# Performance work log

Measured on AMD Instinct MI355X. Metric: run time of the kernel, lower is better.

Reference implementation:

```python
import jax, jax.numpy as jnp
import numpy as np
from jax import lax

B, C, H, W = 4, 256, 64, 64
NH, DK, DV = 8, 32, 32
KER, PAD = 3, 1


def conv1x1(x, w, b=None):
    # x: [B,C,H,W], w: [O,C] (1x1 conv kernel), b: [O] or None
    y = jnp.einsum('bchw,oc->bohw', x, w)
    if b is not None:
        y = y + b[None, :, None, None]
    return y


def unfold(x, k, pad):
    # F.unfold equivalent: [B,C,H,W] -> [B, C*k*k, H, W] (channel-major patch order)
    return lax.conv_general_dilated_patches(x, (k, k), (1, 1), [(pad, pad), (pad, pad)])


def local_attention(q, k, v, kernel, pad, n_head):
    # per-head local windowed attention over a kernel x kernel neighborhood
    b, c, h, w = q.shape
    d = c // n_head
    kk = kernel * kernel
    qh = q.reshape(b, n_head, d, h, w)
    kpat = unfold(k, kernel, pad).reshape(b, n_head, d, kk, h, w)
    vpat = unfold(v, kernel, pad).reshape(b, n_head, d, kk, h, w)
    scale = 1.0 / np.sqrt(float(d)).astype(np.float32)
    logits = jnp.einsum('bhdxy,bhdkxy->bhkxy', qh, kpat) * scale
    attn = jax.nn.softmax(logits, axis=2)
    out = jnp.einsum('bhkxy,bhdkxy->bhdxy', attn, vpat)
    return out.reshape(b, c, h, w)


def layernorm2d(x, g, b, eps=1e-6):
    mu = jnp.mean(x, axis=1, keepdims=True)
    var = jnp.mean((x - mu) ** 2, axis=1, keepdims=True)
    return (x - mu) / jnp.sqrt(var + eps) * g[None, :, None, None] + b[None, :, None, None]


def batchnorm2d(x, g, b, eps=1e-5):
    mu = jnp.mean(x, axis=(0, 2, 3), keepdims=True)
    var = jnp.mean((x - mu) ** 2, axis=(0, 2, 3), keepdims=True)
    return (x - mu) / jnp.sqrt(var + eps) * g[None, :, None, None] + b[None, :, None, None]


def mha(xq, xkv, wq, wk, wv, wfc, g, bias, kernel, pad):
    residual = xq
    q = conv1x1(xq, wq)
    k = conv1x1(xkv, wk)
    v = conv1x1(xkv, wv)
    o = local_attention(q, k, v, kernel, pad, NH)
    o = conv1x1(o, wfc) + residual
    return layernorm2d(o, g, bias)


def ffn(x, w1, b1, w2, b2, g, bias):
    residual = x
    y = conv1x1(jax.nn.relu(conv1x1(x, w1, b1)), w2, b2)
    y = batchnorm2d(y, g, bias)
    return y + residual


def setup_inputs() -> dict:
    key = jax.random.key(0)
    ks = jax.random.split(key, 16)
    s = 0.05
    d = {
        'input1': jax.random.normal(ks[0], (B, C, H, W), jnp.float32),
        'input2': jax.random.normal(ks[1], (B, C, H, W), jnp.float32),
        'slf_wq': jax.random.normal(ks[2], (NH * DK, C), jnp.float32) * s,
        'slf_wk': jax.random.normal(ks[3], (NH * DK, C), jnp.float32) * s,
        'slf_wv': jax.random.normal(ks[4], (NH * DV, C), jnp.float32) * s,
        'slf_fc': jax.random.normal(ks[5], (C, NH * DV), jnp.float32) * s,
        'slf_g': jnp.ones((C,), jnp.float32),
        'slf_b': jnp.zeros((C,), jnp.float32),
        'crs_wq': jax.random.normal(ks[6], (NH * DK, C), jnp.float32) * s,
        'crs_wk': jax.random.normal(ks[7], (NH * DK, C), jnp.float32) * s,
        'crs_wv': jax.random.normal(ks[8], (NH * DV, C), jnp.float32) * s,
        'crs_fc': jax.random.normal(ks[9], (C, NH * DV), jnp.float32) * s,
        'crs_g': jnp.ones((C,), jnp.float32),
        'crs_b': jnp.zeros((C,), jnp.float32),
        'ffn_w1': jax.random.normal(ks[10], (C, C), jnp.float32) * s,
        'ffn_b1': jnp.zeros((C,), jnp.float32),
        'ffn_w2': jax.random.normal(ks[11], (C, C), jnp.float32) * s,
        'ffn_b2': jnp.zeros((C,), jnp.float32),
        'ffn_bn_g': jnp.ones((C,), jnp.float32),
        'ffn_bn_b': jnp.zeros((C,), jnp.float32),
        'kernel': KER,
        'pad': PAD,
    }
    return d


def reference(input1, input2, slf_wq, slf_wk, slf_wv, slf_fc, slf_g, slf_b,
              crs_wq, crs_wk, crs_wv, crs_fc, crs_g, crs_b,
              ffn_w1, ffn_b1, ffn_w2, ffn_b2, ffn_bn_g, ffn_bn_b, kernel, pad):
    slf1 = mha(input1, input1, slf_wq, slf_wk, slf_wv, slf_fc, slf_g, slf_b, kernel, pad)
    slf2 = mha(input2, input2, slf_wq, slf_wk, slf_wv, slf_fc, slf_g, slf_b, kernel, pad)
    crs1 = mha(slf1, slf2, crs_wq, crs_wk, crs_wv, crs_fc, crs_g, crs_b, kernel, pad)
    crs2 = mha(slf2, slf1, crs_wq, crs_wk, crs_wv, crs_fc, crs_g, crs_b, kernel, pad)
    out1 = ffn(crs1, ffn_w1, ffn_b1, ffn_w2, ffn_b2, ffn_bn_g, ffn_bn_b)
    out2 = ffn(crs2, ffn_w1, ffn_b1, ffn_w2, ffn_b2, ffn_bn_g, ffn_bn_b)
    return (out1, out2)
```

## Files before the change

kernel.cpp:

```cpp
#include <hip/hip_runtime.h>
#include <stdint.h>

using u16 = unsigned short;
typedef __bf16 bf16x8 __attribute__((ext_vector_type(8)));
typedef __bf16 bf16x2 __attribute__((ext_vector_type(2)));
typedef float f32x4 __attribute__((ext_vector_type(4)));

#define NPIX 16384
#define CDIM 256

__device__ __forceinline__ float b2f(u16 u) {
  union { unsigned i; float f; } c; c.i = ((unsigned)u) << 16; return c.f;
}
__device__ __forceinline__ u16 f2b(float x) {
  union { __bf16 h; u16 u; } c; c.h = (__bf16)x; return c.u;
}
__device__ __forceinline__ unsigned pack2(float a, float b) {
  union { bf16x2 v; unsigned u; } c; c.v[0] = (__bf16)a; c.v[1] = (__bf16)b; return c.u;
}
__device__ __forceinline__ void unpack8(uint4 w, float* f) {
  f[0] = b2f((u16)(w.x & 0xffffu)); f[1] = b2f((u16)(w.x >> 16));
  f[2] = b2f((u16)(w.y & 0xffffu)); f[3] = b2f((u16)(w.y >> 16));
  f[4] = b2f((u16)(w.z & 0xffffu)); f[5] = b2f((u16)(w.z >> 16));
  f[6] = b2f((u16)(w.w & 0xffffu)); f[7] = b2f((u16)(w.w >> 16));
}

__device__ __forceinline__ void async16(u16* l, const u16* g) {
  __builtin_amdgcn_global_load_lds((const __attribute__((address_space(1))) void*)g,
                                   (__attribute__((address_space(3))) void*)l, 16, 0, 0);
}

template <int NI, int NT>
__device__ __forceinline__ void stage_swz(u16* lds, const u16* src, int tid) {
#pragma unroll
  for (int i = 0; i < NI; ++i) {
    const int idx = i * NT + tid;
    const int row = idx >> 3;
    const int c8 = (idx & 7) ^ (row & 7);
    async16(lds + idx * 8, src + (size_t)row * 256 + c8 * 8);
  }
}

__device__ __forceinline__ void compute_tile(const u16* ab, const u16* bb,
                                             f32x4 (&acc)[4][4], int wr, int wc,
                                             int l15, int l4, int sw) {
#pragma unroll
  for (int kk = 0; kk < 2; ++kk) {
    const int cs = ((kk * 4 + l4) ^ sw) * 8;
    bf16x8 af[4], bfr[4];
#pragma unroll
    for (int mi = 0; mi < 4; ++mi)
      af[mi] = *(const bf16x8*)&ab[(wr * 64 + mi * 16 + l15) * 64 + cs];
#pragma unroll
    for (int ni = 0; ni < 4; ++ni)
      bfr[ni] = *(const bf16x8*)&bb[(wc * 64 + ni * 16 + l15) * 64 + cs];
#pragma unroll
    for (int mi = 0; mi < 4; ++mi)
#pragma unroll
      for (int ni = 0; ni < 4; ++ni)
        acc[mi][ni] = __builtin_amdgcn_mfma_f32_16x16x32_bf16(af[mi], bfr[ni],
                                                              acc[mi][ni], 0, 0, 0);
  }
}

__global__ void prep(const float* __restrict__ x1, const float* __restrict__ x2,
                     u16* __restrict__ X1, u16* __restrict__ X2,
                     const float* s0, const float* s1, const float* s2,
                     const float* s3, const float* s4, const float* s5,
                     const float* s6, const float* s7, const float* s8,
                     const float* s9, u16* __restrict__ wdst,
                     float* __restrict__ stats) {
  const int t = threadIdx.x;
  const int yy = blockIdx.y;
  if (yy >= 32) {
    const int m = yy - 32;
    if (m == 0 && blockIdx.x == 0) {
      ((float4*)stats)[t] = float4{0.f, 0.f, 0.f, 0.f};
    }
    const float* s;
    switch (m) {
      case 0: s = s0; break; case 1: s = s1; break; case 2: s = s2; break;
      case 3: s = s3; break; case 4: s = s4; break; case 5: s = s5; break;
      case 6: s = s6; break; case 7: s = s7; break; case 8: s = s8; break;
      default: s = s9; break;
    }
    const int i = (blockIdx.x * 256 + t) * 4;
    float4 v = *(const float4*)(s + i);
    uint2 o;
    o.x = pack2(v.x, v.y);
    o.y = pack2(v.z, v.w);
    *(uint2*)(wdst + (size_t)m * 65536 + i) = o;
    return;
  }
  __shared__ u16 tile[64][65];
  const int z = yy >> 2;
  const float* x = (z < 4) ? x1 : x2;
  u16* X = (z < 4) ? X1 : X2;
  const int b = z & 3, c0 = (yy & 3) * 64, hw0 = blockIdx.x * 64;
  {
    const int hw_l = t & 63, cb = t >> 6;
#pragma unroll
    for (int i = 0; i < 16; ++i) {
      const int c_l = cb * 16 + i;
      tile[c_l][hw_l] = f2b(x[((size_t)(b * 256 + c0 + c_l)) * 4096 + hw0 + hw_l]);
    }
  }
  __syncthreads();
  {
    const int c_l = t & 63, hb = t >> 6;
#pragma unroll
    for (int i = 0; i < 16; ++i) {
      const int hw_l = hb * 16 + i;
      X[((size_t)(b * 4096 + hw0 + hw_l)) * 256 + c0 + c_l] = tile[c_l][hw_l];
    }
  }
}

struct PG { const u16* X[6]; const u16* W[3]; u16* D[6]; };

__global__ void gemm_qkv(PG a) {
  __shared__ u16 As[2][8192];
  __shared__ u16 Bs[2][8192];
  const int tid = threadIdx.x;
  const int wave = tid >> 6, lane = tid & 63;
  const int p0 = blockIdx.x * 128;
  const int g = blockIdx.y >> 1, o0 = (blockIdx.y & 1) * 128;
  const int z = blockIdx.z;
  const u16* X = a.X[z * 3 + g];
  const u16* W = a.W[g];
  u16* D = a.D[z * 3 + g];
  const int wr = wave & 1, wc = wave >> 1;
  const int l15 = lane & 15, l4 = lane >> 4;
  const int sw = l15 & 7;
  f32x4 acc[4][4] = {};

  const u16* Xp = X + (size_t)p0 * 256;
  const u16* Wp = W + (size_t)o0 * 256;
  stage_swz<4, 256>(As[0], Xp, tid);
  stage_swz<4, 256>(Bs[0], Wp, tid);
  __syncthreads();

  for (int kt = 0; kt < 4; ++kt) {
    const int cur = kt & 1;
    if (kt < 3) {
      stage_swz<4, 256>(As[cur ^ 1], Xp + (kt + 1) * 64, tid);
      stage_swz<4, 256>(Bs[cur ^ 1], Wp + (kt + 1) * 64, tid);
    }
    compute_tile(As[cur], Bs[cur], acc, wr, wc, l15, l4, sw);
    __syncthreads();
  }
#pragma unroll
  for (int ni = 0; ni < 4; ++ni) {
    const int o = o0 + wc * 64 + ni * 16 + l15;
#pragma unroll
    for (int mi = 0; mi < 4; ++mi)
#pragma unroll
      for (int r = 0; r < 4; ++r) {
        const int p = p0 + wr * 64 + mi * 16 + l4 * 4 + r;
        D[(size_t)p * 256 + o] = f2b(acc[mi][ni][r]);
      }
  }
}

struct Paf { const u16* Q[2]; const u16* K[2]; const u16* V[2];
             const u16* res[2]; u16* dst[2];
             const u16* W; const float* g; const float* b; };

__global__ __launch_bounds__(512) void attn_fc_ln(Paf a) {
  __shared__ u16 A4[2][8192];
  __shared__ u16 Bs[16384];
  __shared__ float red[2][128][4];
  const int tid = threadIdx.x;
  const int wave = tid >> 6, lane = tid & 63;
  const int wr = wave & 1, wc = wave >> 1;
  const int l15 = lane & 15, l4 = lane >> 4;
  const int sw = l15 & 7;
  const int p0 = blockIdx.x * 128;
  const int z = blockIdx.y;
  const u16* __restrict__ Q = a.Q[z];
  const u16* __restrict__ K = a.K[z];
  const u16* __restrict__ V = a.V[z];
  const u16* __restrict__ res = a.res[z];
  u16* dst = a.dst[z];

  const int p_l = tid >> 2, hh = tid & 3;
  const int p = p0 + p_l;
  const int yq = (p >> 6) & 63, xq = p & 63;

  bool inb[9];
  ptrdiff_t noff[9];
#pragma unroll
  for (int j = 0; j < 9; ++j) {
    const int dy = j / 3 - 1, dx = j % 3 - 1;
    inb[j] = ((unsigned)(yq + dy) < 64u) && ((unsigned)(xq + dx) < 64u);
    noff[j] = (ptrdiff_t)(dy * 64 + dx) * 256;
  }

  stage_swz<4, 512>(Bs, a.W, tid);
  __builtin_amdgcn_sched_barrier(0);

  f32x4 acc[4][4] = {};
  for (int h = 0; h < 2; ++h) {
    const int head = h * 4 + hh;
    const size_t base = (size_t)p * 256 + head * 32;
    float q[32];
    {
      const uint4* qp = (const uint4*)(Q + base);
#pragma unroll
      for (int i = 0; i < 4; ++i) { uint4 w = qp[i]; unpack8(w, q + i * 8); }
    }
    float accj[9];
#pragma unroll
    for (int j = 0; j < 9; ++j) accj[j] = 0.f;
#pragma unroll
    for (int i = 0; i < 4; ++i) {
      uint4 w[9];
#pragma unroll
      for (int j = 0; j < 9; ++j)
        if (inb[j]) w[j] = ((const uint4*)(K + base + noff[j]))[i];
#pragma unroll
      for (int j = 0; j < 9; ++j) {
        if (inb[j]) {
          float kf[8]; unpack8(w[j], kf);
#pragma unroll
          for (int d = 0; d < 8; ++d) accj[j] += q[i * 8 + d] * kf[d];
        }
      }
    }
    float lg[9];
    float mx = -1e30f;
#pragma unroll
    for (int j = 0; j < 9; ++j) {
      const float l = inb[j] ? accj[j] * 0.17677669529663687f : 0.f;
      lg[j] = l;
      mx = fmaxf(mx, l);
    }
    float pr[9], den = 0.f;
#pragma unroll
    for (int j = 0; j < 9; ++j) { pr[j] = __expf(lg[j] - mx); den += pr[j]; }
    float out[32];
#pragma unroll
    for (int d = 0; d < 32; ++d) out[d] = 0.f;
#pragma unroll
    for (int i = 0; i < 4; ++i) {
      uint4 w[9];
#pragma unroll
      for (int j = 0; j < 9; ++j)
        if (inb[j]) w[j] = ((const uint4*)(V + base + noff[j]))[i];
#pragma unroll
      for (int j = 0; j < 9; ++j) {
        if (inb[j]) {
          float vf[8]; unpack8(w[j], vf);
          const float pw = pr[j];
#pragma unroll
          for (int d = 0; d < 8; ++d) out[i * 8 + d] += pw * vf[d];
        }
      }
    }
    const float inv = 1.f / den;
#pragma unroll
    for (int i = 0; i < 4; ++i) {
      uint4 w;
      w.x = pack2(out[i * 8 + 0] * inv, out[i * 8 + 1] * inv);
      w.y = pack2(out[i * 8 + 2] * inv, out[i * 8 + 3] * inv);
      w.z = pack2(out[i * 8 + 4] * inv, out[i * 8 + 5] * inv);
      w.w = pack2(out[i * 8 + 6] * inv, out[i * 8 + 7] * inv);
      const int c8g = hh * 4 + i;
      const int sub = c8g >> 3, c8in = c8g & 7;
      *(uint4*)&A4[sub][p_l * 64 + ((c8in ^ (p_l & 7)) * 8)] = w;
    }

    __syncthreads();
    compute_tile(A4[0], Bs, acc, wr, wc, l15, l4, sw);
    __syncthreads();
    stage_swz<4, 512>(Bs, a.W + (h * 2 + 1) * 64, tid);
    __syncthreads();
    compute_tile(A4[1], Bs, acc, wr, wc, l15, l4, sw);
    __syncthreads();
    if (h == 0) {
      stage_swz<4, 512>(Bs, a.W + 2 * 64, tid);
      __builtin_amdgcn_sched_barrier(0);
    }
  }

#pragma unroll
  for (int mi = 0; mi < 4; ++mi) {
#pragma unroll
    for (int r = 0; r < 4; ++r) {
      const int pl = wr * 64 + mi * 16 + l4 * 4 + r;
      const int pp = p0 + pl;
      float s = 0.f, s2 = 0.f;
#pragma unroll
      for (int ni = 0; ni < 4; ++ni) {
        const int o = wc * 64 + ni * 16 + l15;
        float vv = acc[mi][ni][r] + b2f(res[(size_t)pp * 256 + o]);
        acc[mi][ni][r] = vv;
        s += vv; s2 += vv * vv;
      }
#pragma unroll
      for (int m = 1; m < 16; m <<= 1) {
        s += __shfl_xor(s, m); s2 += __shfl_xor(s2, m);
      }
      if (l15 == 0) { red[0][pl][wc] = s; red[1][pl][wc] = s2; }
    }
  }
  __syncthreads();

  float gv[4], bv[4];
#pragma unroll
  for (int ni = 0; ni < 4; ++ni) {
    const int o = wc * 64 + ni * 16 + l15;
    gv[ni] = a.g[o]; bv[ni] = a.b[o];
  }
#pragma unroll
  for (int mi = 0; mi < 4; ++mi) {
#pragma unroll
    for (int r = 0; r < 4; ++r) {
      const int pl = wr * 64 + mi * 16 + l4 * 4 + r;
      const float st = red[0][pl][0] + red[0][pl][1] + red[0][pl][2] + red[0][pl][3];
      const float s2t = red[1][pl][0] + red[1][pl][1] + red[1][pl][2] + red[1][pl][3];
      const float mu = st * (1.f / 256.f);
      const float var = s2t * (1.f / 256.f) - mu * mu;
      const float inv = rsqrtf(var + 1e-6f);
      const int pp = p0 + pl;
#pragma unroll
      for (int ni = 0; ni < 4; ++ni) {
        const int o = wc * 64 + ni * 16 + l15;
        dst[(size_t)pp * 256 + o] = f2b((acc[mi][ni][r] - mu) * inv * gv[ni] + bv[ni]);
      }
    }
  }
}

struct Pff { const u16* X[2]; u16* U[2]; float* st[2];
             const u16* W1; const float* b1; const u16* W2; const float* b2; };

__global__ __launch_bounds__(512) void ffn_fused(Pff a) {
  __shared__ u16 mid[4 * 8192];
  __shared__ u16 As[8192];
  __shared__ u16 Bs[16384];
  const int tid = threadIdx.x;
  const int wave = tid >> 6, lane = tid & 63;
  const int wr = wave & 1, wc = wave >> 1;
  const int l15 = lane & 15, l4 = lane >> 4;
  const int sw = l15 & 7;
  const int p0 = blockIdx.x * 128;
  const int z = blockIdx.y;
  const u16* X = a.X[z];
  u16* U = a.U[z];
  float* st = a.st[z];
  const u16* Xp = X + (size_t)p0 * 256;

  f32x4 acc1[4][4] = {};
  for (int kt = 0; kt < 4; ++kt) {
    stage_swz<2, 512>(As, Xp + kt * 64, tid);
    stage_swz<4, 512>(Bs, a.W1 + kt * 64, tid);
    __syncthreads();
    compute_tile(As, Bs, acc1, wr, wc, l15, l4, sw);
    __syncthreads();
  }
  {
    float bvv[4];
#pragma unroll
    for (int ni = 0; ni < 4; ++ni) bvv[ni] = a.b1[wc * 64 + ni * 16 + l15];
    u16* ml = mid + wc * 8192;
#pragma unroll
    for (int mi = 0; mi < 4; ++mi) {
#pragma unroll
      for (int r = 0; r < 4; ++r) {
        const int pl = wr * 64 + mi * 16 + l4 * 4 + r;
#pragma unroll
        for (int ni = 0; ni < 4; ++ni) {
          const int col = ni * 16 + l15;
          const int c8 = col >> 3;
          const u16 hv = f2b(fmaxf(acc1[mi][ni][r] + bvv[ni], 0.f));
          ml[pl * 64 + ((c8 ^ (pl & 7)) * 8) + (col & 7)] = hv;
        }
      }
    }
  }

  f32x4 acc2[4][4] = {};
  for (int kt = 0; kt < 4; ++kt) {
    __syncthreads();
    stage_swz<4, 512>(Bs, a.W2 + kt * 64, tid);
    __syncthreads();
    compute_tile(mid + kt * 8192, Bs, acc2, wr, wc, l15, l4, sw);
  }
#pragma unroll
  for (int ni = 0; ni < 4; ++ni) {
    const int o = wc * 64 + ni * 16 + l15;
    const float bvv = a.b2[o];
    float s = 0.f, s2 = 0.f;
#pragma unroll
    for (int mi = 0; mi < 4; ++mi) {
#pragma unroll
      for (int r = 0; r < 4; ++r) {
        const int p = p0 + wr * 64 + mi * 16 + l4 * 4 + r;
        const u16 hv = f2b(acc2[mi][ni][r] + bvv);
        U[(size_t)p * 256 + o] = hv;
        const float vr = b2f(hv); s += vr; s2 += vr * vr;
      }
    }
    s += __shfl_xor(s, 16); s2 += __shfl_xor(s2, 16);
    s += __shfl_xor(s, 32); s2 += __shfl_xor(s2, 32);
    if (l4 == 0) { atomicAdd(&st[o], s); atomicAdd(&st[256 + o], s2); }
  }
}

struct Pbn { const u16* U[2]; const u16* res[2]; const float* st[2];
             float* out[2]; const float* g; const float* b; };

__global__ void bn_apply(Pbn a) {
  __shared__ float tile[64][65];
  const int t = threadIdx.x;
  const int s = blockIdx.z >> 2, b = blockIdx.z & 3;
  const u16* __restrict__ U = a.U[s];
  const u16* __restrict__ res = a.res[s];
  const float* st = a.st[s];
  float* out = a.out[s];
  const int c0 = blockIdx.y * 64, hw0 = blockIdx.x * 64;
  {
    const int c_l = t & 63, hb = t >> 6;
    const int c = c0 + c_l;
    const float mu = st[c] * (1.f / 16384.f);
    const float var = st[256 + c] * (1.f / 16384.f) - mu * mu;
    const float sc = rsqrtf(var + 1e-5f) * a.g[c];
    const float sh = a.b[c] - mu * sc;
#pragma unroll
    for (int i = 0; i < 16; ++i) {
      const int hw_l = hb * 16 + i;
      const size_t p = (size_t)b * 4096 + hw0 + hw_l;
      const float u = b2f(U[p * 256 + c]);
      const float r = b2f(res[p * 256 + c]);
      tile[hw_l][c_l] = u * sc + sh + r;
    }
  }
  __syncthreads();
  {
    const int hw_l = t & 63, cb2 = t >> 6;
#pragma unroll
    for (int i = 0; i < 16; ++i) {
      const int c_l = cb2 * 16 + i;
      out[((size_t)(b * 256 + c0 + c_l)) * 4096 + hw0 + hw_l] = tile[hw_l][c_l];
    }
  }
}

extern "C" void kernel_launch(void* const* d_in, const int* in_sizes, int n_in,
                              void* d_out, int out_size, void* d_ws, size_t ws_size,
                              hipStream_t stream) {
  const float* input1 = (const float*)d_in[0];
  const float* input2 = (const float*)d_in[1];
  const float* slf_wq = (const float*)d_in[2];
  const float* slf_wk = (const float*)d_in[3];
  const float* slf_wv = (const float*)d_in[4];
  const float* slf_fc = (const float*)d_in[5];
  const float* slf_g  = (const float*)d_in[6];
  const float* slf_b  = (const float*)d_in[7];
  const float* crs_wq = (const float*)d_in[8];
  const float* crs_wk = (const float*)d_in[9];
  const float* crs_wv = (const float*)d_in[10];
  const float* crs_fc = (const float*)d_in[11];
  const float* crs_g  = (const float*)d_in[12];
  const float* crs_b  = (const float*)d_in[13];
  const float* ffn_w1 = (const float*)d_in[14];
  const float* ffn_b1 = (const float*)d_in[15];
  const float* ffn_w2 = (const float*)d_in[16];
  const float* ffn_b2 = (const float*)d_in[17];
  const float* bn_g   = (const float*)d_in[18];
  const float* bn_b   = (const float*)d_in[19];

  float* out = (float*)d_out;
  u16* ws = (u16*)d_ws;
  const size_t TS = (size_t)NPIX * CDIM;
  u16* b[10];
  for (int i = 0; i < 10; ++i) b[i] = ws + (size_t)i * TS;
  u16* wb = ws + 10 * TS;
  u16 *Wsq = wb,             *Wsk = wb + 65536,     *Wsv = wb + 2 * 65536,
      *Wsf = wb + 3 * 65536, *Wcq = wb + 4 * 65536, *Wck = wb + 5 * 65536,
      *Wcv = wb + 6 * 65536, *Wcf = wb + 7 * 65536, *W1 = wb + 8 * 65536,
      *W2 = wb + 9 * 65536;
  float* stats = (float*)(wb + 10 * 65536);

  const dim3 tb(256);

  prep<<<dim3(64, 42), tb, 0, stream>>>(input1, input2, b[0], b[1],
                                        slf_wq, slf_wk, slf_wv, slf_fc,
                                        crs_wq, crs_wk, crs_wv, crs_fc,
                                        ffn_w1, ffn_w2, wb, stats);

  PG sa;
  sa.X[0] = b[0]; sa.X[1] = b[0]; sa.X[2] = b[0];
  sa.X[3] = b[1]; sa.X[4] = b[1]; sa.X[5] = b[1];
  sa.W[0] = Wsq; sa.W[1] = Wsk; sa.W[2] = Wsv;
  sa.D[0] = b[4]; sa.D[1] = b[5]; sa.D[2] = b[6];
  sa.D[3] = b[7]; sa.D[4] = b[8]; sa.D[5] = b[9];
  gemm_qkv<<<dim3(NPIX / 128, 6, 2), tb, 0, stream>>>(sa);

  Paf f1;
  f1.Q[0] = b[4]; f1.K[0] = b[5]; f1.V[0] = b[6];
  f1.Q[1] = b[7]; f1.K[1] = b[8]; f1.V[1] = b[9];
  f1.res[0] = b[0]; f1.res[1] = b[1];
  f1.dst[0] = b[2]; f1.dst[1] = b[3];
  f1.W = Wsf; f1.g = slf_g; f1.b = slf_b;
  attn_fc_ln<<<dim3(NPIX / 128, 2), dim3(512), 0, stream>>>(f1);

  PG ca;
  ca.X[0] = b[2]; ca.X[1] = b[3]; ca.X[2] = b[3];
  ca.X[3] = b[3]; ca.X[4] = b[2]; ca.X[5] = b[2];
  ca.W[0] = Wcq; ca.W[1] = Wck; ca.W[2] = Wcv;
  ca.D[0] = b[4]; ca.D[1] = b[5]; ca.D[2] = b[6];
  ca.D[3] = b[7]; ca.D[4] = b[8]; ca.D[5] = b[9];
  gemm_qkv<<<dim3(NPIX / 128, 6, 2), tb, 0, stream>>>(ca);

  Paf f2;
  f2.Q[0] = b[4]; f2.K[0] = b[5]; f2.V[0] = b[6];
  f2.Q[1] = b[7]; f2.K[1] = b[8]; f2.V[1] = b[9];
  f2.res[0] = b[2]; f2.res[1] = b[3];
  f2.dst[0] = b[0]; f2.dst[1] = b[1];
  f2.W = Wcf; f2.g = crs_g; f2.b = crs_b;
  attn_fc_ln<<<dim3(NPIX / 128, 2), dim3(512), 0, stream>>>(f2);

  Pff ff;
  ff.X[0] = b[0]; ff.X[1] = b[1];
  ff.U[0] = b[4]; ff.U[1] = b[7];
  ff.st[0] = stats; ff.st[1] = stats + 512;
  ff.W1 = W1; ff.b1 = ffn_b1; ff.W2 = W2; ff.b2 = ffn_b2;
  ffn_fused<<<dim3(NPIX / 128, 2), dim3(512), 0, stream>>>(ff);

  Pbn bn;
  bn.U[0] = b[4]; bn.U[1] = b[7];
  bn.res[0] = b[0]; bn.res[1] = b[1];
  bn.st[0] = stats; bn.st[1] = stats + 512;
  bn.out[0] = out; bn.out[1] = out + TS;
  bn.g = bn_g; bn.b = bn_b;
  bn_apply<<<dim3(64, 4, 8), tb, 0, stream>>>(bn);
}
```

Baseline: 286.5 us.

## Fuse cross-attention Q projection into self-attn and FFN into cross-attn

```diff
diff --git a/kernel.cpp b/kernel.cpp
--- a/kernel.cpp
+++ b/kernel.cpp
@@ -118,6 +118,7 @@
 
 struct PG { const u16* X[6]; const u16* W[3]; u16* D[6]; };
 
+template <int NG>
 __global__ void gemm_qkv(PG a) {
   __shared__ u16 As[2][8192];
   __shared__ u16 Bs[2][8192];
@@ -126,9 +127,9 @@
   const int p0 = blockIdx.x * 128;
   const int g = blockIdx.y >> 1, o0 = (blockIdx.y & 1) * 128;
   const int z = blockIdx.z;
-  const u16* X = a.X[z * 3 + g];
+  const u16* X = a.X[z * NG + g];
   const u16* W = a.W[g];
-  u16* D = a.D[z * 3 + g];
+  u16* D = a.D[z * NG + g];
   const int wr = wave & 1, wc = wave >> 1;
   const int l15 = lane & 15, l4 = lane >> 4;
   const int sw = l15 & 7;
@@ -162,13 +163,14 @@
   }
 }
 
-struct Paf { const u16* Q[2]; const u16* K[2]; const u16* V[2];
-             const u16* res[2]; u16* dst[2];
-             const u16* W; const float* g; const float* b; };
-
-__global__ __launch_bounds__(512) void attn_fc_ln(Paf a) {
+struct Pas { const u16* Q[2]; const u16* K[2]; const u16* V[2];
+             const u16* res[2]; u16* dstS[2]; u16* dstQc[2];
+             const u16* Wfc; const u16* Wcq; const float* g; const float* b; };
+
+__global__ __launch_bounds__(512) void attn_s(Pas a) {
   __shared__ u16 A4[2][8192];
   __shared__ u16 Bs[16384];
+  __shared__ u16 S4[4][8192];
   __shared__ float red[2][128][4];
   const int tid = threadIdx.x;
   const int wave = tid >> 6, lane = tid & 63;
@@ -181,7 +183,8 @@
   const u16* __restrict__ K = a.K[z];
   const u16* __restrict__ V = a.V[z];
   const u16* __restrict__ res = a.res[z];
-  u16* dst = a.dst[z];
+  u16* dstS = a.dstS[z];
+  u16* dstQc = a.dstQc[z];
 
   const int p_l = tid >> 2, hh = tid & 3;
   const int p = p0 + p_l;
@@ -196,7 +199,7 @@
     noff[j] = (ptrdiff_t)(dy * 64 + dx) * 256;
   }
 
-  stage_swz<4, 512>(Bs, a.W, tid);
+  stage_swz<4, 512>(Bs, a.Wfc, tid);
   __builtin_amdgcn_sched_barrier(0);
 
   f32x4 acc[4][4] = {};
@@ -273,15 +276,18 @@
     __syncthreads();
     compute_tile(A4[0], Bs, acc, wr, wc, l15, l4, sw);
     __syncthreads();
-    stage_swz<4, 512>(Bs, a.W + (h * 2 + 1) * 64, tid);
+    stage_swz<4, 512>(Bs, a.Wfc + (h * 2 + 1) * 64, tid);
     __syncthreads();
     compute_tile(A4[1], Bs, acc, wr, wc, l15, l4, sw);
     __syncthreads();
     if (h == 0) {
-      stage_swz<4, 512>(Bs, a.W + 2 * 64, tid);
+      stage_swz<4, 512>(Bs, a.Wfc + 2 * 64, tid);
       __builtin_amdgcn_sched_barrier(0);
     }
   }
+
+  stage_swz<4, 512>(Bs, a.Wcq, tid);
+  __builtin_amdgcn_sched_barrier(0);
 
 #pragma unroll
   for (int mi = 0; mi < 4; ++mi) {
@@ -326,19 +332,46 @@
 #pragma unroll
       for (int ni = 0; ni < 4; ++ni) {
         const int o = wc * 64 + ni * 16 + l15;
-        dst[(size_t)pp * 256 + o] = f2b((acc[mi][ni][r] - mu) * inv * gv[ni] + bv[ni]);
-      }
-    }
-  }
-}
-
-struct Pff { const u16* X[2]; u16* U[2]; float* st[2];
-             const u16* W1; const float* b1; const u16* W2; const float* b2; };
-
-__global__ __launch_bounds__(512) void ffn_fused(Pff a) {
-  __shared__ u16 mid[4 * 8192];
-  __shared__ u16 As[8192];
+        const u16 hv = f2b((acc[mi][ni][r] - mu) * inv * gv[ni] + bv[ni]);
+        dstS[(size_t)pp * 256 + o] = hv;
+        const int c8 = (ni * 16 + l15) >> 3;
+        S4[wc][pl * 64 + ((c8 ^ (pl & 7)) * 8) + (l15 & 7)] = hv;
+      }
+    }
+  }
+  __syncthreads();
+
+  u16* a4f = &A4[0][0];
+  f32x4 accq[4][4] = {};
+  for (int kt = 0; kt < 4; ++kt) {
+    if (kt < 3)
+      stage_swz<4, 512>(((kt + 1) & 1) ? a4f : Bs, a.Wcq + (kt + 1) * 64, tid);
+    compute_tile(&S4[kt][0], (kt & 1) ? a4f : Bs, accq, wr, wc, l15, l4, sw);
+    __syncthreads();
+  }
+#pragma unroll
+  for (int ni = 0; ni < 4; ++ni) {
+    const int o = wc * 64 + ni * 16 + l15;
+#pragma unroll
+    for (int mi = 0; mi < 4; ++mi)
+#pragma unroll
+      for (int r = 0; r < 4; ++r) {
+        const int pp = p0 + wr * 64 + mi * 16 + l4 * 4 + r;
+        dstQc[(size_t)pp * 256 + o] = f2b(accq[mi][ni][r]);
+      }
+  }
+}
+
+struct Pcf { const u16* Q[2]; const u16* K[2]; const u16* V[2];
+             const u16* resS[2]; u16* dstC[2]; u16* U[2]; float* st[2];
+             const u16* Wfc; const float* g; const float* b;
+             const u16* W1; const float* bb1; const u16* W2; const float* bb2; };
+
+__global__ __launch_bounds__(512) void attn_c_ffn(Pcf a) {
+  __shared__ u16 A4[2][8192];
   __shared__ u16 Bs[16384];
+  __shared__ u16 M4[4][8192];
+  __shared__ float red[2][128][4];
   const int tid = threadIdx.x;
   const int wave = tid >> 6, lane = tid & 63;
   const int wr = wave & 1, wc = wave >> 1;
@@ -346,24 +379,184 @@
   const int sw = l15 & 7;
   const int p0 = blockIdx.x * 128;
   const int z = blockIdx.y;
-  const u16* X = a.X[z];
+  const u16* __restrict__ Q = a.Q[z];
+  const u16* __restrict__ K = a.K[z];
+  const u16* __restrict__ V = a.V[z];
+  const u16* __restrict__ resS = a.resS[z];
+  u16* dstC = a.dstC[z];
   u16* U = a.U[z];
   float* st = a.st[z];
-  const u16* Xp = X + (size_t)p0 * 256;
-
+
+  const int p_l = tid >> 2, hh = tid & 3;
+  const int p = p0 + p_l;
+  const int yq = (p >> 6) & 63, xq = p & 63;
+
+  bool inb[9];
+  ptrdiff_t noff[9];
+#pragma unroll
+  for (int j = 0; j < 9; ++j) {
+    const int dy = j / 3 - 1, dx = j % 3 - 1;
+    inb[j] = ((unsigned)(yq + dy) < 64u) && ((unsigned)(xq + dx) < 64u);
+    noff[j] = (ptrdiff_t)(dy * 64 + dx) * 256;
+  }
+
+  stage_swz<4, 512>(Bs, a.Wfc, tid);
+  __builtin_amdgcn_sched_barrier(0);
+
+  f32x4 acc[4][4] = {};
+  for (int h = 0; h < 2; ++h) {
+    const int head = h * 4 + hh;
+    const size_t base = (size_t)p * 256 + head * 32;
+    float q[32];
+    {
+      const uint4* qp = (const uint4*)(Q + base);
+#pragma unroll
+      for (int i = 0; i < 4; ++i) { uint4 w = qp[i]; unpack8(w, q + i * 8); }
+    }
+    float accj[9];
+#pragma unroll
+    for (int j = 0; j < 9; ++j) accj[j] = 0.f;
+#pragma unroll
+    for (int i = 0; i < 4; ++i) {
+      uint4 w[9];
+#pragma unroll
+      for (int j = 0; j < 9; ++j)
+        if (inb[j]) w[j] = ((const uint4*)(K + base + noff[j]))[i];
+#pragma unroll
+      for (int j = 0; j < 9; ++j) {
+        if (inb[j]) {
+          float kf[8]; unpack8(w[j], kf);
+#pragma unroll
+          for (int d = 0; d < 8; ++d) accj[j] += q[i * 8 + d] * kf[d];
+        }
+      }
+    }
+    float lg[9];
+    float mx = -1e30f;
+#pragma unroll
+    for (int j = 0; j < 9; ++j) {
+      const float l = inb[j] ? accj[j] * 0.17677669529663687f : 0.f;
+      lg[j] = l;
+      mx = fmaxf(mx, l);
+    }
+    float pr[9], den = 0.f;
+#pragma unroll
+    for (int j = 0; j < 9; ++j) { pr[j] = __expf(lg[j] - mx); den += pr[j]; }
+    float out[32];
+#pragma unroll
+    for (int d = 0; d < 32; ++d) out[d] = 0.f;
+#pragma unroll
+    for (int i = 0; i < 4; ++i) {
+      uint4 w[9];
+#pragma unroll
+      for (int j = 0; j < 9; ++j)
+        if (inb[j]) w[j] = ((const uint4*)(V + base + noff[j]))[i];
+#pragma unroll
+      for (int j = 0; j < 9; ++j) {
+        if (inb[j]) {
+          float vf[8]; unpack8(w[j], vf);
+          const float pw = pr[j];
+#pragma unroll
+          for (int d = 0; d < 8; ++d) out[i * 8 + d] += pw * vf[d];
+        }
+      }
+    }
+    const float inv = 1.f / den;
+#pragma unroll
+    for (int i = 0; i < 4; ++i) {
+      uint4 w;
+      w.x = pack2(out[i * 8 + 0] * inv, out[i * 8 + 1] * inv);
+      w.y = pack2(out[i * 8 + 2] * inv, out[i * 8 + 3] * inv);
+      w.z = pack2(out[i * 8 + 4] * inv, out[i * 8 + 5] * inv);
+      w.w = pack2(out[i * 8 + 6] * inv, out[i * 8 + 7] * inv);
+      const int c8g = hh * 4 + i;
+      const int sub = c8g >> 3, c8in = c8g & 7;
+      *(uint4*)&A4[sub][p_l * 64 + ((c8in ^ (p_l & 7)) * 8)] = w;
+    }
+
+    __syncthreads();
+    compute_tile(A4[0], Bs, acc, wr, wc, l15, l4, sw);
+    __syncthreads();
+    stage_swz<4, 512>(Bs, a.Wfc + (h * 2 + 1) * 64, tid);
+    __syncthreads();
+    compute_tile(A4[1], Bs, acc, wr, wc, l15, l4, sw);
+    __syncthreads();
+    if (h == 0) {
+      stage_swz<4, 512>(Bs, a.Wfc + 2 * 64, tid);
+      __builtin_amdgcn_sched_barrier(0);
+    }
+  }
+
+  stage_swz<4, 512>(Bs, a.W1, tid);
+  __builtin_amdgcn_sched_barrier(0);
+
+#pragma unroll
+  for (int mi = 0; mi < 4; ++mi) {
+#pragma unroll
+    for (int r = 0; r < 4; ++r) {
+      const int pl = wr * 64 + mi * 16 + l4 * 4 + r;
+      const int pp = p0 + pl;
+      float s = 0.f, s2 = 0.f;
+#pragma unroll
+      for (int ni = 0; ni < 4; ++ni) {
+        const int o = wc * 64 + ni * 16 + l15;
+        float vv = acc[mi][ni][r] + b2f(resS[(size_t)pp * 256 + o]);
+        acc[mi][ni][r] = vv;
+        s += vv; s2 += vv * vv;
+      }
+#pragma unroll
+      for (int m = 1; m < 16; m <<= 1) {
+        s += __shfl_xor(s, m); s2 += __shfl_xor(s2, m);
+      }
+      if (l15 == 0) { red[0][pl][wc] = s; red[1][pl][wc] = s2; }
+    }
+  }
+  __syncthreads();
+
+  float gv[4], bv[4];
+#pragma unroll
+  for (int ni = 0; ni < 4; ++ni) {
+    const int o = wc * 64 + ni * 16 + l15;
+    gv[ni] = a.g[o]; bv[ni] = a.b[o];
+  }
+#pragma unroll
+  for (int mi = 0; mi < 4; ++mi) {
+#pragma unroll
+    for (int r = 0; r < 4; ++r) {
+      const int pl = wr * 64 + mi * 16 + l4 * 4 + r;
+      const float st2 = red[0][pl][0] + red[0][pl][1] + red[0][pl][2] + red[0][pl][3];
+      const float s2t = red[1][pl][0] + red[1][pl][1] + red[1][pl][2] + red[1][pl][3];
+      const float mu = st2 * (1.f / 256.f);
+      const float var = s2t * (1.f / 256.f) - mu * mu;
+      const float inv = rsqrtf(var + 1e-6f);
+      const int pp = p0 + pl;
+#pragma unroll
+      for (int ni = 0; ni < 4; ++ni) {
+        const int o = wc * 64 + ni * 16 + l15;
+        const u16 hv = f2b((acc[mi][ni][r] - mu) * inv * gv[ni] + bv[ni]);
+        dstC[(size_t)pp * 256 + o] = hv;
+        const int c8 = (ni * 16 + l15) >> 3;
+        M4[wc][pl * 64 + ((c8 ^ (pl & 7)) * 8) + (l15 & 7)] = hv;
+      }
+    }
+  }
+  __syncthreads();
+
+  u16* a4f = &A4[0][0];
   f32x4 acc1[4][4] = {};
   for (int kt = 0; kt < 4; ++kt) {
-    stage_swz<2, 512>(As, Xp + kt * 64, tid);
-    stage_swz<4, 512>(Bs, a.W1 + kt * 64, tid);
-    __syncthreads();
-    compute_tile(As, Bs, acc1, wr, wc, l15, l4, sw);
-    __syncthreads();
-  }
+    if (kt < 3)
+      stage_swz<4, 512>(((kt + 1) & 1) ? a4f : Bs, a.W1 + (kt + 1) * 64, tid);
+    compute_tile(&M4[kt][0], (kt & 1) ? a4f : Bs, acc1, wr, wc, l15, l4, sw);
+    __syncthreads();
+  }
+  stage_swz<4, 512>(Bs, a.W2, tid);
+  __builtin_amdgcn_sched_barrier(0);
   {
     float bvv[4];
 #pragma unroll
-    for (int ni = 0; ni < 4; ++ni) bvv[ni] = a.b1[wc * 64 + ni * 16 + l15];
-    u16* ml = mid + wc * 8192;
+    for (int ni = 0; ni < 4; ++ni) bvv[ni] = a.bb1[wc * 64 + ni * 16 + l15];
+    u16* ml = &M4[wc][0];
 #pragma unroll
     for (int mi = 0; mi < 4; ++mi) {
 #pragma unroll
@@ -379,26 +572,27 @@
       }
     }
   }
+  __syncthreads();
 
   f32x4 acc2[4][4] = {};
   for (int kt = 0; kt < 4; ++kt) {
-    __syncthreads();
-    stage_swz<4, 512>(Bs, a.W2 + kt * 64, tid);
-    __syncthreads();
-    compute_tile(mid + kt * 8192, Bs, acc2, wr, wc, l15, l4, sw);
+    if (kt < 3)
+      stage_swz<4, 512>(((kt + 1) & 1) ? a4f : Bs, a.W2 + (kt + 1) * 64, tid);
+    compute_tile(&M4[kt][0], (kt & 1) ? a4f : Bs, acc2, wr, wc, l15, l4, sw);
+    __syncthreads();
   }
 #pragma unroll
   for (int ni = 0; ni < 4; ++ni) {
     const int o = wc * 64 + ni * 16 + l15;
-    const float bvv = a.b2[o];
+    const float bvv = a.bb2[o];
     float s = 0.f, s2 = 0.f;
 #pragma unroll
     for (int mi = 0; mi < 4; ++mi) {
 #pragma unroll
       for (int r = 0; r < 4; ++r) {
-        const int p = p0 + wr * 64 + mi * 16 + l4 * 4 + r;
+        const int pp = p0 + wr * 64 + mi * 16 + l4 * 4 + r;
         const u16 hv = f2b(acc2[mi][ni][r] + bvv);
-        U[(size_t)p * 256 + o] = hv;
+        U[(size_t)pp * 256 + o] = hv;
         const float vr = b2f(hv); s += vr; s2 += vr * vr;
       }
     }
@@ -496,41 +690,40 @@
   sa.W[0] = Wsq; sa.W[1] = Wsk; sa.W[2] = Wsv;
   sa.D[0] = b[4]; sa.D[1] = b[5]; sa.D[2] = b[6];
   sa.D[3] = b[7]; sa.D[4] = b[8]; sa.D[5] = b[9];
-  gemm_qkv<<<dim3(NPIX / 128, 6, 2), tb, 0, stream>>>(sa);
-
-  Paf f1;
+  gemm_qkv<3><<<dim3(NPIX / 128, 6, 2), tb, 0, stream>>>(sa);
+
+  Pas f1;
   f1.Q[0] = b[4]; f1.K[0] = b[5]; f1.V[0] = b[6];
   f1.Q[1] = b[7]; f1.K[1] = b[8]; f1.V[1] = b[9];
   f1.res[0] = b[0]; f1.res[1] = b[1];
-  f1.dst[0] = b[2]; f1.dst[1] = b[3];
-  f1.W = Wsf; f1.g = slf_g; f1.b = slf_b;
-  attn_fc_ln<<<dim3(NPIX / 128, 2), dim3(512), 0, stream>>>(f1);
+  f1.dstS[0] = b[2]; f1.dstS[1] = b[3];
+  f1.dstQc[0] = b[4]; f1.dstQc[1] = b[7];
+  f1.Wfc = Wsf; f1.Wcq = Wcq; f1.g = slf_g; f1.b = slf_b;
+  attn_s<<<dim3(NPIX / 128, 2), dim3(512), 0, stream>>>(f1);
 
   PG ca;
-  ca.X[0] = b[2]; ca.X[1] = b[3]; ca.X[2] = b[3];
-  ca.X[3] = b[3]; ca.X[4] = b[2]; ca.X[5] = b[2];
-  ca.W[0] = Wcq; ca.W[1] = Wck; ca.W[2] = Wcv;
-  ca.D[0] = b[4]; ca.D[1] = b[5]; ca.D[2] = b[6];
-  ca.D[3] = b[7]; ca.D[4] = b[8]; ca.D[5] = b[9];
-  gemm_qkv<<<dim3(NPIX / 128, 6, 2), tb, 0, stream>>>(ca);
-
-  Paf f2;
-  f2.Q[0] = b[4]; f2.K[0] = b[5]; f2.V[0] = b[6];
-  f2.Q[1] = b[7]; f2.K[1] = b[8]; f2.V[1] = b[9];
-  f2.res[0] = b[2]; f2.res[1] = b[3];
-  f2.dst[0] = b[0]; f2.dst[1] = b[1];
-  f2.W = Wcf; f2.g = crs_g; f2.b = crs_b;
-  attn_fc_ln<<<dim3(NPIX / 128, 2), dim3(512), 0, stream>>>(f2);
-
-  Pff ff;
-  ff.X[0] = b[0]; ff.X[1] = b[1];
-  ff.U[0] = b[4]; ff.U[1] = b[7];
-  ff.st[0] = stats; ff.st[1] = stats + 512;
-  ff.W1 = W1; ff.b1 = ffn_b1; ff.W2 = W2; ff.b2 = ffn_b2;
-  ffn_fused<<<dim3(NPIX / 128, 2), dim3(512), 0, stream>>>(ff);
+  ca.X[0] = b[2]; ca.X[1] = b[2];
+  ca.X[2] = b[3]; ca.X[3] = b[3];
+  ca.X[4] = nullptr; ca.X[5] = nullptr;
+  ca.W[0] = Wck; ca.W[1] = Wcv; ca.W[2] = nullptr;
+  ca.D[0] = b[5]; ca.D[1] = b[6];
+  ca.D[2] = b[8]; ca.D[3] = b[9];
+  ca.D[4] = nullptr; ca.D[5] = nullptr;
+  gemm_qkv<2><<<dim3(NPIX / 128, 4, 2), tb, 0, stream>>>(ca);
+
+  Pcf f2;
+  f2.Q[0] = b[4]; f2.K[0] = b[8]; f2.V[0] = b[9];
+  f2.Q[1] = b[7]; f2.K[1] = b[5]; f2.V[1] = b[6];
+  f2.resS[0] = b[2]; f2.resS[1] = b[3];
+  f2.dstC[0] = b[0]; f2.dstC[1] = b[1];
+  f2.U[0] = b[2]; f2.U[1] = b[3];
+  f2.st[0] = stats; f2.st[1] = stats + 512;
+  f2.Wfc = Wcf; f2.g = crs_g; f2.b = crs_b;
+  f2.W1 = W1; f2.bb1 = ffn_b1; f2.W2 = W2; f2.bb2 = ffn_b2;
+  attn_c_ffn<<<dim3(NPIX / 128, 2), dim3(512), 0, stream>>>(f2);
 
   Pbn bn;
-  bn.U[0] = b[4]; bn.U[1] = b[7];
+  bn.U[0] = b[2]; bn.U[1] = b[3];
   bn.res[0] = b[0]; bn.res[1] = b[1];
   bn.st[0] = stats; bn.st[1] = stats + 512;
   bn.out[0] = out; bn.out[1] = out + TS;
```

Result: no change. 283.0 us (-1.2%).
